# Kernel tuning notes

Measured on AMD Instinct MI355X. Metric: run time of the kernel, lower is better.

The kernel has to match this reference:

```python
import jax, jax.numpy as jnp
import numpy as np

N_NODES = 100000
IN_DIM = 128
HID = 64
OUT = 5
N_EDGES = 3200000


def setup_inputs() -> dict:
    key = jax.random.key(0)
    ks = jax.random.split(key, 10)
    x = jax.random.normal(ks[0], (N_NODES, IN_DIM), dtype=jnp.float32)
    edge_index = jax.random.randint(ks[1], (2, N_EDGES), 0, N_NODES, dtype=jnp.int64)
    def glorot(k, shape):
        lim = (6.0 / (shape[0] + shape[1])) ** 0.5
        return jax.random.uniform(k, shape, dtype=jnp.float32, minval=-lim, maxval=lim)
    # SAGEConv: lin_l (on aggregated neighbors, with bias), lin_r (on root, no bias)
    W1l = glorot(ks[2], (HID, IN_DIM)); b1l = jnp.zeros((HID,), jnp.float32)
    W1r = glorot(ks[3], (HID, IN_DIM))
    W2l = glorot(ks[4], (HID, HID)); b2l = jnp.zeros((HID,), jnp.float32)
    W2r = glorot(ks[5], (HID, HID))
    Wh = glorot(ks[6], (OUT, HID)); bh = jnp.zeros((OUT,), jnp.float32)
    return {"x": x, "edge_index": edge_index, "W1l": W1l, "b1l": b1l, "W1r": W1r,
            "W2l": W2l, "b2l": b2l, "W2r": W2r, "Wh": Wh, "bh": bh}


def _sage_conv(x, src, dst, Wl, bl, Wr):
    # mean-aggregate source features at destination nodes, then linear
    msg = x[src]                                            # [E, d]
    s = jax.ops.segment_sum(msg, dst, num_segments=N_NODES)  # [N, d]
    cnt = jax.ops.segment_sum(jnp.ones((src.shape[0],), x.dtype), dst,
                              num_segments=N_NODES)
    mean = s / jnp.maximum(cnt, 1.0)[:, None]
    return mean @ Wl.T + bl + x @ Wr.T


def reference(x, edge_index, W1l, b1l, W1r, W2l, b2l, W2r, Wh, bh):
    src, dst = edge_index[0], edge_index[1]
    h = jax.nn.relu(_sage_conv(x, src, dst, W1l, b1l, W1r))
    h = jax.nn.relu(_sage_conv(h, src, dst, W2l, b2l, W2r))
    logits = h @ Wh.T + bh
    return (logits, h)
```

## Files before the change

### kernel.cpp

```cpp
#include <hip/hip_runtime.h>

#define N_NODES 100000
#define IN_DIM 128
#define HID 64
#define OUT_DIM 5
#define N_EDGES 3200000

#define BSHIFT 7
#define BROWS 128
#define NBUCK ((N_NODES + BROWS - 1) / BROWS)
#define FILLB_CHUNK 16384
#define NBF ((N_EDGES + FILLB_CHUNK - 1) / FILLB_CHUNK)

typedef __attribute__((ext_vector_type(8))) short short8;
typedef __attribute__((ext_vector_type(8))) unsigned short ushort8_t;
typedef __attribute__((ext_vector_type(4))) float f32x4;
typedef __attribute__((ext_vector_type(2))) float f32x2_t;
typedef unsigned short ushort_t;
typedef unsigned int uint_t;
typedef unsigned char uchar_t;

static __device__ inline ushort_t f2bf(float f) {
  union { float f; uint_t u; } v; v.f = f;
  const uint_t r = v.u + 0x7FFFu + ((v.u >> 16) & 1u);
  return (ushort_t)(r >> 16);
}
static __device__ inline uint_t pack2(float a, float b) {
  return (uint_t)f2bf(a) | ((uint_t)f2bf(b) << 16);
}
static __device__ inline float bf2f(ushort_t u) {
  return __uint_as_float((uint_t)u << 16);
}
static __device__ inline void fp8x4_acc(uint_t w, float& c0, float& c1, float& c2,
                                        float& c3) {
  const f32x2_t lo = __builtin_amdgcn_cvt_pk_f32_fp8((int)w, false);
  const f32x2_t hi = __builtin_amdgcn_cvt_pk_f32_fp8((int)w, true);
  c0 += lo[0];
  c1 += lo[1];
  c2 += hi[0];
  c3 += hi[1];
}
static __device__ inline uchar_t f2fp8(float f) {
  return (uchar_t)__builtin_amdgcn_cvt_pk_fp8_f32(f, 0.0f, 0, false);
}

__global__ __launch_bounds__(256) void histA_k(const int* __restrict__ dst,
                                               int* __restrict__ H) {
  __shared__ int hist[NBUCK];
  const int t = threadIdx.x;
  const int b = blockIdx.x;
  const int e0 = b * FILLB_CHUNK;
  const int e1 = min(e0 + FILLB_CHUNK, N_EDGES);
  for (int i = t; i < NBUCK; i += 256) hist[i] = 0;
  __syncthreads();
  for (int e = e0 + t; e < e1; e += 256) atomicAdd(&hist[dst[e] >> BSHIFT], 1);
  __syncthreads();
  for (int c = t; c < NBUCK; c += 256) H[(size_t)c * NBF + b] = hist[c];
}

__global__ __launch_bounds__(256) void colscan_k(const int* __restrict__ H,
                                                 int* __restrict__ P,
                                                 int* __restrict__ bcount) {
  const int lane = threadIdx.x & 63;
  const int wv = threadIdx.x >> 6;
  const int c = blockIdx.x * 4 + wv;
  if (c >= NBUCK) return;
  const int* col = H + (size_t)c * NBF;
  int* pcol = P + (size_t)c * NBF;
  int carry = 0;
#pragma unroll
  for (int k = 0; k < (NBF + 63) / 64; ++k) {
    const int idx = k * 64 + lane;
    const int v = (idx < NBF) ? col[idx] : 0;
    int s = v;
#pragma unroll
    for (int off = 1; off < 64; off <<= 1) {
      const int x = __shfl_up(s, off);
      if (lane >= off) s += x;
    }
    if (idx < NBF) pcol[idx] = carry + s - v;
    carry += __shfl(s, 63);
  }
  if (lane == 0) bcount[c] = carry;
}

__global__ __launch_bounds__(256) void bscan_k(const int* __restrict__ bcount,
                                               int* __restrict__ boff,
                                               int* __restrict__ noff) {
  __shared__ int pref[NBUCK + 1];
  __shared__ int tsum[256];
  const int t = threadIdx.x;
  int v[4];
  int s = 0;
#pragma unroll
  for (int j = 0; j < 4; ++j) {
    const int idx = t * 4 + j;
    v[j] = (idx < NBUCK) ? bcount[idx] : 0;
    s += v[j];
  }
  tsum[t] = s;
  __syncthreads();
  for (int off = 1; off < 256; off <<= 1) {
    int x = (t >= off) ? tsum[t - off] : 0;
    __syncthreads();
    tsum[t] += x;
    __syncthreads();
  }
  int pre = tsum[t] - s;
#pragma unroll
  for (int j = 0; j < 4; ++j) {
    const int idx = t * 4 + j;
    if (idx < NBUCK) pref[idx] = pre;
    pre += v[j];
  }
  if (t == 0) pref[NBUCK] = N_EDGES;
  __syncthreads();
  for (int i = t; i <= NBUCK; i += 256) boff[i] = pref[i];
  if (t == 0) noff[N_NODES] = N_EDGES;
}

__global__ __launch_bounds__(256) void fillD_k(const int* __restrict__ src,
                                               const int* __restrict__ dst,
                                               const int* __restrict__ boff,
                                               const int* __restrict__ P,
                                               int* __restrict__ bedge) {
  __shared__ int base[NBUCK];
  __shared__ int cur[NBUCK];
  const int t = threadIdx.x;
  const int b = blockIdx.x;
  const int e0 = b * FILLB_CHUNK;
  const int e1 = min(e0 + FILLB_CHUNK, N_EDGES);
  for (int c = t; c < NBUCK; c += 256) {
    base[c] = boff[c] + P[(size_t)c * NBF + b];
    cur[c] = 0;
  }
  __syncthreads();
  for (int e = e0 + t; e < e1; e += 256) {
    const int d = dst[e];
    const int c = d >> BSHIFT;
    const int pos = base[c] + atomicAdd(&cur[c], 1);
    bedge[pos] = (src[e] << BSHIFT) | (d & (BROWS - 1));
  }
}

__global__ __launch_bounds__(256) void csrfill_k(const int* __restrict__ boff,
                                                 const int* __restrict__ bedge,
                                                 int* __restrict__ csr,
                                                 int* __restrict__ noff) {
  __shared__ int hist[BROWS];
  __shared__ int sc[BROWS];
  __shared__ int cur[BROWS];
  const int t = threadIdx.x;
  const int b = blockIdx.x;
  const int e0 = boff[b];
  const int e1 = boff[b + 1];
  if (t < BROWS) {
    hist[t] = 0;
    cur[t] = 0;
  }
  __syncthreads();
  for (int e = e0 + t; e < e1; e += 256) atomicAdd(&hist[bedge[e] & (BROWS - 1)], 1);
  __syncthreads();
  if (t < BROWS) sc[t] = hist[t];
  __syncthreads();
  for (int off = 1; off < BROWS; off <<= 1) {
    int x = (t >= off && t < BROWS) ? sc[t - off] : 0;
    __syncthreads();
    if (t < BROWS) sc[t] += x;
    __syncthreads();
  }
  if (t < BROWS) {
    const int node = b * BROWS + t;
    if (node < N_NODES) noff[node] = e0 + sc[t] - hist[t];
    sc[t] -= hist[t];
  }
  __syncthreads();
  for (int e = e0 + t; e < e1; e += 256) {
    const int p = bedge[e];
    const int d = p & (BROWS - 1);
    const int pos = e0 + sc[d] + atomicAdd(&cur[d], 1);
    csr[pos] = p >> BSHIFT;
  }
}

template <int K, bool BF16IN>
__global__ __launch_bounds__(256) void gemm_mfma(const void* __restrict__ Xv,
                                                 const float* __restrict__ Wl,
                                                 const float* __restrict__ Wr,
                                                 uchar_t* __restrict__ Y8,
                                                 ushort_t* __restrict__ Zb, int n) {
  __shared__ uint4 ldsq[(256 * K * 2) / 16];
  char* xlds = (char*)ldsq;
  char* wlds = xlds + 128 * K * 2;
  const int t = threadIdx.x;
  const int lane = t & 63;
  const int wv = t >> 6;
  const int rowBase = blockIdx.x * 128;
  const int K2 = K * 2;
  const int KC = K / 8;

  for (int c = t; c < 128 * KC; c += 256) {
    const int r = c / KC, k8 = c - r * KC;
    const int row = rowBase + r;
    uint4 w = {0u, 0u, 0u, 0u};
    if (row < n) {
      if (BF16IN) {
        w = ((const uint4*)((const ushort_t*)Xv + (size_t)row * K))[k8];
      } else {
        const float4* p = (const float4*)((const float*)Xv + (size_t)row * K + k8 * 8);
        const float4 f0 = p[0];
        const float4 f1 = p[1];
        w.x = pack2(f0.x, f0.y);
        w.y = pack2(f0.z, f0.w);
        w.z = pack2(f1.x, f1.y);
        w.w = pack2(f1.z, f1.w);
      }
    }
    const int byte = (r * K2 + k8 * 16) ^ ((r & 7) << 4);
    *(uint4*)(xlds + byte) = w;
  }
  for (int c = t; c < 2 * 64 * KC; c += 256) {
    const int m = c / (64 * KC);
    const int c2 = c - m * 64 * KC;
    const int r = c2 / KC, k8 = c2 - r * KC;
    const float4* p = (const float4*)((m ? Wr : Wl) + (size_t)r * K + k8 * 8);
    const float4 f0 = p[0];
    const float4 f1 = p[1];
    uint4 w;
    w.x = pack2(f0.x, f0.y);
    w.y = pack2(f0.z, f0.w);
    w.z = pack2(f1.x, f1.y);
    w.w = pack2(f1.z, f1.w);
    const int byte = (m * 64 * K2) + ((r * K2 + k8 * 16) ^ ((r & 7) << 4));
    *(uint4*)(wlds + byte) = w;
  }
  __syncthreads();

  f32x4 accY[2][4], accZ[2][4];
#pragma unroll
  for (int rt = 0; rt < 2; ++rt)
#pragma unroll
    for (int ct = 0; ct < 4; ++ct) {
      accY[rt][ct] = (f32x4){0.f, 0.f, 0.f, 0.f};
      accZ[rt][ct] = (f32x4){0.f, 0.f, 0.f, 0.f};
    }

  const int fr = lane & 15;
  const int kg = lane >> 4;
#pragma unroll
  for (int kk = 0; kk < K / 32; ++kk) {
    const int kbyte = kk * 64 + kg * 16;
    short8 a[2];
#pragma unroll
    for (int rt = 0; rt < 2; ++rt) {
      const int r = wv * 32 + rt * 16 + fr;
      a[rt] = *(const short8*)(xlds + ((r * K2 + kbyte) ^ ((r & 7) << 4)));
    }
#pragma unroll
    for (int ct = 0; ct < 4; ++ct) {
      const int wr = ct * 16 + fr;
      const int byteY = (wr * K2 + kbyte) ^ ((wr & 7) << 4);
      const short8 bY = *(const short8*)(wlds + byteY);
      const short8 bZ = *(const short8*)(wlds + byteY + 64 * K2);
#pragma unroll
      for (int rt = 0; rt < 2; ++rt) {
        accY[rt][ct] =
            __builtin_amdgcn_mfma_f32_16x16x32_bf16(a[rt], bY, accY[rt][ct], 0, 0, 0);
        accZ[rt][ct] =
            __builtin_amdgcn_mfma_f32_16x16x32_bf16(a[rt], bZ, accZ[rt][ct], 0, 0, 0);
      }
    }
  }

#pragma unroll
  for (int rt = 0; rt < 2; ++rt) {
#pragma unroll
    for (int q = 0; q < 4; ++q) {
      const int row = rowBase + wv * 32 + rt * 16 + kg * 4 + q;
      if (row < n) {
#pragma unroll
        for (int ct = 0; ct < 4; ++ct) {
          const int col = ct * 16 + fr;
          Y8[(size_t)row * 64 + col] = f2fp8(accY[rt][ct][q]);
          Zb[(size_t)row * 64 + col] = f2bf(accZ[rt][ct][q]);
        }
      }
    }
  }
}

template <bool FINAL>
__global__ __launch_bounds__(256) void gather_k(
    const int* __restrict__ noff, const int* __restrict__ csr,
    const uchar_t* __restrict__ Y8, const ushort_t* __restrict__ Zb,
    const float* __restrict__ bias, const float* __restrict__ Wh,
    const float* __restrict__ bh, ushort_t* __restrict__ Hb,
    float* __restrict__ Hf, float* __restrict__ logits, int n) {
  const int lane = threadIdx.x & 63;
  const int g = lane >> 3;
  const int r = lane & 7;
  const int wid = (blockIdx.x * blockDim.x + threadIdx.x) >> 6;
  const int nw = (gridDim.x * blockDim.x) >> 6;
  const float4 biasA = ((const float4*)bias)[2 * r];
  const float4 biasB = ((const float4*)bias)[2 * r + 1];
  float4 whA[5], whB[5];
  if (FINAL) {
#pragma unroll
    for (int o = 0; o < 5; ++o) {
      whA[o] = ((const float4*)(Wh + o * 64))[2 * r];
      whB[o] = ((const float4*)(Wh + o * 64))[2 * r + 1];
    }
  }

  for (int row = wid; row < n; row += nw) {
    const int e0 = noff[row];
    const int e1 = noff[row + 1];
    const int ne = e1 - e0;
    float a0 = 0.f, a1 = 0.f, a2 = 0.f, a3 = 0.f;
    float a4 = 0.f, a5 = 0.f, a6 = 0.f, a7 = 0.f;
    for (int eb = e0; eb < e1; eb += 64) {
      const int eidx = eb + 8 * r + g;
      const int sidx = (eidx < e1) ? csr[eidx] : N_NODES;
      const int msteps = min(8, (e1 - eb + 7) >> 3);
      int j = 0;
      for (; j + 3 < msteps; j += 4) {
        const int s0 = __shfl(sidx, j, 8);
        const int s1 = __shfl(sidx, j + 1, 8);
        const int s2 = __shfl(sidx, j + 2, 8);
        const int s3 = __shfl(sidx, j + 3, 8);
        const uint2 v0 = *(const uint2*)(Y8 + (size_t)s0 * 64 + r * 8);
        const uint2 v1 = *(const uint2*)(Y8 + (size_t)s1 * 64 + r * 8);
        const uint2 v2 = *(const uint2*)(Y8 + (size_t)s2 * 64 + r * 8);
        const uint2 v3 = *(const uint2*)(Y8 + (size_t)s3 * 64 + r * 8);
        fp8x4_acc(v0.x, a0, a1, a2, a3);
        fp8x4_acc(v0.y, a4, a5, a6, a7);
        fp8x4_acc(v1.x, a0, a1, a2, a3);
        fp8x4_acc(v1.y, a4, a5, a6, a7);
        fp8x4_acc(v2.x, a0, a1, a2, a3);
        fp8x4_acc(v2.y, a4, a5, a6, a7);
        fp8x4_acc(v3.x, a0, a1, a2, a3);
        fp8x4_acc(v3.y, a4, a5, a6, a7);
      }
      for (; j < msteps; ++j) {
        const int s0 = __shfl(sidx, j, 8);
        const uint2 v0 = *(const uint2*)(Y8 + (size_t)s0 * 64 + r * 8);
        fp8x4_acc(v0.x, a0, a1, a2, a3);
        fp8x4_acc(v0.y, a4, a5, a6, a7);
      }
    }
#pragma unroll
    for (int d = 8; d <= 32; d <<= 1) {
      a0 += __shfl_xor(a0, d);
      a1 += __shfl_xor(a1, d);
      a2 += __shfl_xor(a2, d);
      a3 += __shfl_xor(a3, d);
      a4 += __shfl_xor(a4, d);
      a5 += __shfl_xor(a5, d);
      a6 += __shfl_xor(a6, d);
      a7 += __shfl_xor(a7, d);
    }

    if (g == 0) {
      const float inv = 1.0f / fmaxf((float)ne, 1.0f);
      const ushort8_t zv = *(const ushort8_t*)(Zb + (size_t)row * 64 + r * 8);
      const float h0 = fmaxf(fmaf(a0, inv, biasA.x + bf2f(zv[0])), 0.0f);
      const float h1 = fmaxf(fmaf(a1, inv, biasA.y + bf2f(zv[1])), 0.0f);
      const float h2 = fmaxf(fmaf(a2, inv, biasA.z + bf2f(zv[2])), 0.0f);
      const float h3 = fmaxf(fmaf(a3, inv, biasA.w + bf2f(zv[3])), 0.0f);
      const float h4 = fmaxf(fmaf(a4, inv, biasB.x + bf2f(zv[4])), 0.0f);
      const float h5 = fmaxf(fmaf(a5, inv, biasB.y + bf2f(zv[5])), 0.0f);
      const float h6 = fmaxf(fmaf(a6, inv, biasB.z + bf2f(zv[6])), 0.0f);
      const float h7 = fmaxf(fmaf(a7, inv, biasB.w + bf2f(zv[7])), 0.0f);
      if (!FINAL) {
        ushort8_t hb;
        hb[0] = f2bf(h0); hb[1] = f2bf(h1); hb[2] = f2bf(h2); hb[3] = f2bf(h3);
        hb[4] = f2bf(h4); hb[5] = f2bf(h5); hb[6] = f2bf(h6); hb[7] = f2bf(h7);
        *(ushort8_t*)(Hb + (size_t)row * 64 + r * 8) = hb;
      } else {
        float4 hfA, hfB;
        hfA.x = h0; hfA.y = h1; hfA.z = h2; hfA.w = h3;
        hfB.x = h4; hfB.y = h5; hfB.z = h6; hfB.w = h7;
        ((float4*)Hf)[(size_t)row * 16 + 2 * r] = hfA;
        ((float4*)Hf)[(size_t)row * 16 + 2 * r + 1] = hfB;
        float q[5];
#pragma unroll
        for (int o = 0; o < 5; ++o) {
          q[o] = h0 * whA[o].x + h1 * whA[o].y + h2 * whA[o].z + h3 * whA[o].w +
                 h4 * whB[o].x + h5 * whB[o].y + h6 * whB[o].z + h7 * whB[o].w;
#pragma unroll
          for (int d = 1; d < 8; d <<= 1) q[o] += __shfl_xor(q[o], d, 8);
        }
        if (r == 0) {
#pragma unroll
          for (int o = 0; o < 5; ++o) logits[(size_t)row * 5 + o] = q[o] + bh[o];
        }
      }
    }
  }
}

extern "C" void kernel_launch(void* const* d_in, const int* in_sizes, int n_in,
                              void* d_out, int out_size, void* d_ws, size_t ws_size,
                              hipStream_t stream) {
  const float* x = (const float*)d_in[0];
  const int* edge = (const int*)d_in[1];
  const float* W1l = (const float*)d_in[2];
  const float* b1l = (const float*)d_in[3];
  const float* W1r = (const float*)d_in[4];
  const float* W2l = (const float*)d_in[5];
  const float* b2l = (const float*)d_in[6];
  const float* W2r = (const float*)d_in[7];
  const float* Wh = (const float*)d_in[8];
  const float* bh = (const float*)d_in[9];
  const int* src = edge;
  const int* dst = edge + N_EDGES;

  float* out = (float*)d_out;
  float* logits = out;
  float* hout = out + (size_t)N_NODES * OUT_DIM;

  const size_t N64 = (size_t)N_NODES * 64;
  ushort_t* zb = (ushort_t*)d_ws;
  ushort_t* h1b = zb + N64;
  uchar_t* y8 = (uchar_t*)(h1b + N64);
  int* H = (int*)(y8 + N64 + 64);
  int* P = H + (size_t)NBUCK * NBF;
  int* bcount = P + (size_t)NBUCK * NBF;
  int* boff = bcount + NBUCK;
  int* bedge = boff + NBUCK + 1;
  int* csr = bedge + N_EDGES;
  int* noff = csr + N_EDGES;

  hipMemsetAsync(y8 + N64, 0, 64, stream);
  histA_k<<<NBF, 256, 0, stream>>>(dst, H);
  colscan_k<<<(NBUCK + 3) / 4, 256, 0, stream>>>(H, P, bcount);
  bscan_k<<<1, 256, 0, stream>>>(bcount, boff, noff);
  fillD_k<<<NBF, 256, 0, stream>>>(src, dst, boff, P, bedge);
  csrfill_k<<<NBUCK, 256, 0, stream>>>(boff, bedge, csr, noff);

  const int mblocks = (N_NODES + 127) / 128;
  const int wblocks = 6250;

  gemm_mfma<IN_DIM, false><<<mblocks, 256, 0, stream>>>(x, W1l, W1r, y8, zb, N_NODES);
  gather_k<false><<<wblocks, 256, 0, stream>>>(noff, csr, y8, zb, b1l, nullptr,
                                               nullptr, h1b, nullptr, nullptr,
                                               N_NODES);

  gemm_mfma<HID, true><<<mblocks, 256, 0, stream>>>(h1b, W2l, W2r, y8, zb, N_NODES);
  gather_k<true><<<wblocks, 256, 0, stream>>>(noff, csr, y8, zb, b2l, Wh, bh,
                                              nullptr, hout, logits, N_NODES);
}
```

Measured before the change: 257.0 us.

## Split neighbor gather into two source-half passes for cache locality

The CSR build now sorts each destination's neighbors by whether the source index lies in the lower or upper half of the node range, and records a split offset per node. Each aggregation is then done in two passes, each touching only half of the source feature table, so the random fp8 gathers are meant to fit better in cache. The first pass writes partial sums in bf16 to a new workspace buffer, and the second pass adds them back before finishing. Non-temporal loads and stores are used for streaming data. The cost is two extra kernel launches, an extra round trip of partial sums, and bf16 rounding of those partials.

Measured after the change: 378.8 us. 47.4% more time.

```diff
diff --git a/kernel.cpp b/kernel.cpp
--- a/kernel.cpp
+++ b/kernel.cpp
@@ -1,6 +1,7 @@
 #include <hip/hip_runtime.h>
 
 #define N_NODES 100000
+#define HALFN 50000
 #define IN_DIM 128
 #define HID 64
 #define OUT_DIM 5
@@ -146,39 +147,46 @@
 __global__ __launch_bounds__(256) void csrfill_k(const int* __restrict__ boff,
                                                  const int* __restrict__ bedge,
                                                  int* __restrict__ csr,
-                                                 int* __restrict__ noff) {
-  __shared__ int hist[BROWS];
-  __shared__ int sc[BROWS];
-  __shared__ int cur[BROWS];
+                                                 int* __restrict__ noff,
+                                                 int* __restrict__ nsplit) {
+  __shared__ int hist[256];
+  __shared__ int sc[256];
+  __shared__ int cur[256];
   const int t = threadIdx.x;
   const int b = blockIdx.x;
   const int e0 = boff[b];
   const int e1 = boff[b + 1];
-  if (t < BROWS) {
-    hist[t] = 0;
-    cur[t] = 0;
-  }
-  __syncthreads();
-  for (int e = e0 + t; e < e1; e += 256) atomicAdd(&hist[bedge[e] & (BROWS - 1)], 1);
-  __syncthreads();
-  if (t < BROWS) sc[t] = hist[t];
-  __syncthreads();
-  for (int off = 1; off < BROWS; off <<= 1) {
-    int x = (t >= off && t < BROWS) ? sc[t - off] : 0;
+  hist[t] = 0;
+  cur[t] = 0;
+  __syncthreads();
+  for (int e = e0 + t; e < e1; e += 256) {
+    const int p = bedge[e];
+    const int key = ((p & (BROWS - 1)) << 1) | ((p >> BSHIFT) >= HALFN ? 1 : 0);
+    atomicAdd(&hist[key], 1);
+  }
+  __syncthreads();
+  sc[t] = hist[t];
+  __syncthreads();
+  for (int off = 1; off < 256; off <<= 1) {
+    int x = (t >= off) ? sc[t - off] : 0;
     __syncthreads();
-    if (t < BROWS) sc[t] += x;
+    sc[t] += x;
     __syncthreads();
   }
+  sc[t] -= hist[t];
+  __syncthreads();
   if (t < BROWS) {
     const int node = b * BROWS + t;
-    if (node < N_NODES) noff[node] = e0 + sc[t] - hist[t];
-    sc[t] -= hist[t];
+    if (node < N_NODES) {
+      noff[node] = e0 + sc[2 * t];
+      nsplit[node] = e0 + sc[2 * t + 1];
+    }
   }
   __syncthreads();
   for (int e = e0 + t; e < e1; e += 256) {
     const int p = bedge[e];
-    const int d = p & (BROWS - 1);
-    const int pos = e0 + sc[d] + atomicAdd(&cur[d], 1);
+    const int key = ((p & (BROWS - 1)) << 1) | ((p >> BSHIFT) >= HALFN ? 1 : 0);
+    const int pos = e0 + sc[key] + atomicAdd(&cur[key], 1);
     csr[pos] = p >> BSHIFT;
   }
 }
@@ -289,20 +297,24 @@
   }
 }
 
-template <bool FINAL>
+template <int PHASE, bool FINAL>
 __global__ __launch_bounds__(256) void gather_k(
-    const int* __restrict__ noff, const int* __restrict__ csr,
-    const uchar_t* __restrict__ Y8, const ushort_t* __restrict__ Zb,
-    const float* __restrict__ bias, const float* __restrict__ Wh,
-    const float* __restrict__ bh, ushort_t* __restrict__ Hb,
+    const int* __restrict__ noff, const int* __restrict__ nsplit,
+    const int* __restrict__ csr, const uchar_t* __restrict__ Y8,
+    const ushort_t* __restrict__ Zb, const float* __restrict__ bias,
+    const float* __restrict__ Wh, const float* __restrict__ bh,
+    ushort_t* __restrict__ Pacc, ushort_t* __restrict__ Hb,
     float* __restrict__ Hf, float* __restrict__ logits, int n) {
   const int lane = threadIdx.x & 63;
   const int g = lane >> 3;
   const int r = lane & 7;
   const int wid = (blockIdx.x * blockDim.x + threadIdx.x) >> 6;
   const int nw = (gridDim.x * blockDim.x) >> 6;
-  const float4 biasA = ((const float4*)bias)[2 * r];
-  const float4 biasB = ((const float4*)bias)[2 * r + 1];
+  float4 biasA = {0, 0, 0, 0}, biasB = {0, 0, 0, 0};
+  if (PHASE == 1) {
+    biasA = ((const float4*)bias)[2 * r];
+    biasB = ((const float4*)bias)[2 * r + 1];
+  }
   float4 whA[5], whB[5];
   if (FINAL) {
 #pragma unroll
@@ -313,14 +325,22 @@
   }
 
   for (int row = wid; row < n; row += nw) {
-    const int e0 = noff[row];
-    const int e1 = noff[row + 1];
-    const int ne = e1 - e0;
+    int e0, e1, ne = 0;
+    if (PHASE == 0) {
+      e0 = __builtin_nontemporal_load(noff + row);
+      e1 = __builtin_nontemporal_load(nsplit + row);
+    } else {
+      const int n0 = __builtin_nontemporal_load(noff + row);
+      e0 = __builtin_nontemporal_load(nsplit + row);
+      e1 = __builtin_nontemporal_load(noff + row + 1);
+      ne = e1 - n0;
+    }
     float a0 = 0.f, a1 = 0.f, a2 = 0.f, a3 = 0.f;
     float a4 = 0.f, a5 = 0.f, a6 = 0.f, a7 = 0.f;
     for (int eb = e0; eb < e1; eb += 64) {
       const int eidx = eb + 8 * r + g;
-      const int sidx = (eidx < e1) ? csr[eidx] : N_NODES;
+      const int sidx =
+          (eidx < e1) ? __builtin_nontemporal_load(csr + eidx) : N_NODES;
       const int msteps = min(8, (e1 - eb + 7) >> 3);
       int j = 0;
       for (; j + 3 < msteps; j += 4) {
@@ -361,38 +381,53 @@
     }
 
     if (g == 0) {
-      const float inv = 1.0f / fmaxf((float)ne, 1.0f);
-      const ushort8_t zv = *(const ushort8_t*)(Zb + (size_t)row * 64 + r * 8);
-      const float h0 = fmaxf(fmaf(a0, inv, biasA.x + bf2f(zv[0])), 0.0f);
-      const float h1 = fmaxf(fmaf(a1, inv, biasA.y + bf2f(zv[1])), 0.0f);
-      const float h2 = fmaxf(fmaf(a2, inv, biasA.z + bf2f(zv[2])), 0.0f);
-      const float h3 = fmaxf(fmaf(a3, inv, biasA.w + bf2f(zv[3])), 0.0f);
-      const float h4 = fmaxf(fmaf(a4, inv, biasB.x + bf2f(zv[4])), 0.0f);
-      const float h5 = fmaxf(fmaf(a5, inv, biasB.y + bf2f(zv[5])), 0.0f);
-      const float h6 = fmaxf(fmaf(a6, inv, biasB.z + bf2f(zv[6])), 0.0f);
-      const float h7 = fmaxf(fmaf(a7, inv, biasB.w + bf2f(zv[7])), 0.0f);
-      if (!FINAL) {
-        ushort8_t hb;
-        hb[0] = f2bf(h0); hb[1] = f2bf(h1); hb[2] = f2bf(h2); hb[3] = f2bf(h3);
-        hb[4] = f2bf(h4); hb[5] = f2bf(h5); hb[6] = f2bf(h6); hb[7] = f2bf(h7);
-        *(ushort8_t*)(Hb + (size_t)row * 64 + r * 8) = hb;
+      if (PHASE == 0) {
+        ushort8_t pb;
+        pb[0] = f2bf(a0); pb[1] = f2bf(a1); pb[2] = f2bf(a2); pb[3] = f2bf(a3);
+        pb[4] = f2bf(a4); pb[5] = f2bf(a5); pb[6] = f2bf(a6); pb[7] = f2bf(a7);
+        __builtin_nontemporal_store(pb, (ushort8_t*)(Pacc + (size_t)row * 64 + r * 8));
       } else {
-        float4 hfA, hfB;
-        hfA.x = h0; hfA.y = h1; hfA.z = h2; hfA.w = h3;
-        hfB.x = h4; hfB.y = h5; hfB.z = h6; hfB.w = h7;
-        ((float4*)Hf)[(size_t)row * 16 + 2 * r] = hfA;
-        ((float4*)Hf)[(size_t)row * 16 + 2 * r + 1] = hfB;
-        float q[5];
-#pragma unroll
-        for (int o = 0; o < 5; ++o) {
-          q[o] = h0 * whA[o].x + h1 * whA[o].y + h2 * whA[o].z + h3 * whA[o].w +
-                 h4 * whB[o].x + h5 * whB[o].y + h6 * whB[o].z + h7 * whB[o].w;
-#pragma unroll
-          for (int d = 1; d < 8; d <<= 1) q[o] += __shfl_xor(q[o], d, 8);
-        }
-        if (r == 0) {
-#pragma unroll
-          for (int o = 0; o < 5; ++o) logits[(size_t)row * 5 + o] = q[o] + bh[o];
+        const ushort8_t pb = __builtin_nontemporal_load(
+            (const ushort8_t*)(Pacc + (size_t)row * 64 + r * 8));
+        a0 += bf2f(pb[0]); a1 += bf2f(pb[1]); a2 += bf2f(pb[2]); a3 += bf2f(pb[3]);
+        a4 += bf2f(pb[4]); a5 += bf2f(pb[5]); a6 += bf2f(pb[6]); a7 += bf2f(pb[7]);
+        const float inv = 1.0f / fmaxf((float)ne, 1.0f);
+        const ushort8_t zv = __builtin_nontemporal_load(
+            (const ushort8_t*)(Zb + (size_t)row * 64 + r * 8));
+        const float h0 = fmaxf(fmaf(a0, inv, biasA.x + bf2f(zv[0])), 0.0f);
+        const float h1 = fmaxf(fmaf(a1, inv, biasA.y + bf2f(zv[1])), 0.0f);
+        const float h2 = fmaxf(fmaf(a2, inv, biasA.z + bf2f(zv[2])), 0.0f);
+        const float h3 = fmaxf(fmaf(a3, inv, biasA.w + bf2f(zv[3])), 0.0f);
+        const float h4 = fmaxf(fmaf(a4, inv, biasB.x + bf2f(zv[4])), 0.0f);
+        const float h5 = fmaxf(fmaf(a5, inv, biasB.y + bf2f(zv[5])), 0.0f);
+        const float h6 = fmaxf(fmaf(a6, inv, biasB.z + bf2f(zv[6])), 0.0f);
+        const float h7 = fmaxf(fmaf(a7, inv, biasB.w + bf2f(zv[7])), 0.0f);
+        if (!FINAL) {
+          ushort8_t hb;
+          hb[0] = f2bf(h0); hb[1] = f2bf(h1); hb[2] = f2bf(h2); hb[3] = f2bf(h3);
+          hb[4] = f2bf(h4); hb[5] = f2bf(h5); hb[6] = f2bf(h6); hb[7] = f2bf(h7);
+          __builtin_nontemporal_store(hb,
+                                      (ushort8_t*)(Hb + (size_t)row * 64 + r * 8));
+        } else {
+          f32x4 hfA = {h0, h1, h2, h3};
+          f32x4 hfB = {h4, h5, h6, h7};
+          __builtin_nontemporal_store(hfA,
+                                      (f32x4*)(Hf + (size_t)row * 64 + r * 8));
+          __builtin_nontemporal_store(hfB,
+                                      (f32x4*)(Hf + (size_t)row * 64 + r * 8 + 4));
+          float q[5];
+#pragma unroll
+          for (int o = 0; o < 5; ++o) {
+            q[o] = h0 * whA[o].x + h1 * whA[o].y + h2 * whA[o].z + h3 * whA[o].w +
+                   h4 * whB[o].x + h5 * whB[o].y + h6 * whB[o].z + h7 * whB[o].w;
+#pragma unroll
+            for (int d = 1; d < 8; d <<= 1) q[o] += __shfl_xor(q[o], d, 8);
+          }
+          if (r == 0) {
+#pragma unroll
+            for (int o = 0; o < 5; ++o)
+              __builtin_nontemporal_store(q[o] + bh[o], logits + (size_t)row * 5 + o);
+          }
         }
       }
     }
@@ -422,7 +457,8 @@
   const size_t N64 = (size_t)N_NODES * 64;
   ushort_t* zb = (ushort_t*)d_ws;
   ushort_t* h1b = zb + N64;
-  uchar_t* y8 = (uchar_t*)(h1b + N64);
+  ushort_t* pacc = h1b + N64;
+  uchar_t* y8 = (uchar_t*)(pacc + N64);
   int* H = (int*)(y8 + N64 + 64);
   int* P = H + (size_t)NBUCK * NBF;
   int* bcount = P + (size_t)NBUCK * NBF;
@@ -430,23 +466,31 @@
   int* bedge = boff + NBUCK + 1;
   int* csr = bedge + N_EDGES;
   int* noff = csr + N_EDGES;
+  int* nsplit = noff + N_NODES + 1;
 
   hipMemsetAsync(y8 + N64, 0, 64, stream);
   histA_k<<<NBF, 256, 0, stream>>>(dst, H);
   colscan_k<<<(NBUCK + 3) / 4, 256, 0, stream>>>(H, P, bcount);
   bscan_k<<<1, 256, 0, stream>>>(bcount, boff, noff);
   fillD_k<<<NBF, 256, 0, stream>>>(src, dst, boff, P, bedge);
-  csrfill_k<<<NBUCK, 256, 0, stream>>>(boff, bedge, csr, noff);
+  csrfill_k<<<NBUCK, 256, 0, stream>>>(boff, bedge, csr, noff, nsplit);
 
   const int mblocks = (N_NODES + 127) / 128;
   const int wblocks = 6250;
 
   gemm_mfma<IN_DIM, false><<<mblocks, 256, 0, stream>>>(x, W1l, W1r, y8, zb, N_NODES);
-  gather_k<false><<<wblocks, 256, 0, stream>>>(noff, csr, y8, zb, b1l, nullptr,
-                                               nullptr, h1b, nullptr, nullptr,
-                                               N_NODES);
+  gather_k<0, false><<<wblocks, 256, 0, stream>>>(noff, nsplit, csr, y8, nullptr,
+                                                  nullptr, nullptr, nullptr, pacc,
+                                                  nullptr, nullptr, nullptr, N_NODES);
+  gather_k<1, false><<<wblocks, 256, 0, stream>>>(noff, nsplit, csr, y8, zb, b1l,
+                                                  nullptr, nullptr, pacc, h1b,
+                                                  nullptr, nullptr, N_NODES);
 
   gemm_mfma<HID, true><<<mblocks, 256, 0, stream>>>(h1b, W2l, W2r, y8, zb, N_NODES);
-  gather_k<true><<<wblocks, 256, 0, stream>>>(noff, csr, y8, zb, b2l, Wh, bh,
-                                              nullptr, hout, logits, N_NODES);
-}
+  gather_k<0, false><<<wblocks, 256, 0, stream>>>(noff, nsplit, csr, y8, nullptr,
+                                                  nullptr, nullptr, nullptr, pacc,
+                                                  nullptr, nullptr, nullptr, N_NODES);
+  gather_k<1, true><<<wblocks, 256, 0, stream>>>(noff, nsplit, csr, y8, zb, b2l, Wh,
+                                                 bh, pacc, nullptr, hout, logits,
+                                                 N_NODES);
+}
```
